# Optimization experiments

Measured on AMD Instinct MI355X. Metric: run time of the kernel, lower is better.

The kernel has to match this reference:

```python
import jax, jax.numpy as jnp
import numpy as np

IN_SZ, HID_SZ, OUT_SZ, NUM_HEAD = 64, 128, 64, 16
BATCH = 131072


def setup_inputs() -> dict:
    key = jax.random.key(0)
    ks = jax.random.split(key, 5)
    # PyTorch Linear default init: U(-1/sqrt(fan_in), 1/sqrt(fan_in))
    b1lim = 1.0 / np.sqrt(IN_SZ)
    b2lim = 1.0 / np.sqrt(HID_SZ)
    return {
        "x": jax.random.normal(ks[0], (BATCH, IN_SZ), dtype=jnp.float32),
        "W1": jax.random.uniform(ks[1], (NUM_HEAD, IN_SZ, HID_SZ), jnp.float32, -b1lim, b1lim),
        "b1": jax.random.uniform(ks[2], (NUM_HEAD, HID_SZ), jnp.float32, -b1lim, b1lim),
        "W2": jax.random.uniform(ks[3], (NUM_HEAD, HID_SZ, OUT_SZ), jnp.float32, -b2lim, b2lim),
        "b2": jax.random.uniform(ks[4], (NUM_HEAD, OUT_SZ), jnp.float32, -b2lim, b2lim),
    }


def reference(x, W1, b1, W2, b2):
    # All heads as one grouped matmul: [B,in] x [H,in,hid] -> [B,H,hid]
    h = jnp.einsum("bi,hio->bho", x, W1) + b1[None, :, :]
    h = jax.nn.elu(h)
    # [B,H,hid] x [H,hid,out] -> [B,H,out]  (matches torch.stack(...).transpose(0,1))
    out = jnp.einsum("bho,hos->bhs", h, W2) + b2[None, :, :]
    return out
```

## Files before the change

kernel.cpp:

```cpp
#include <hip/hip_runtime.h>
#include <hip/hip_bf16.h>


typedef __attribute__((ext_vector_type(8))) short bf16x8;
typedef __attribute__((ext_vector_type(4))) float f32x4;
typedef __attribute__((ext_vector_type(4))) unsigned int u32x4;

union frag_u { u32x4 u; bf16x8 b; };

#define MFMA16(A, B, C) __builtin_amdgcn_mfma_f32_16x16x32_bf16((A), (B), (C), 0, 0, 0)

__device__ __forceinline__ void split2(float a, float b, unsigned &wh, unsigned &wl) {
  unsigned ua = __float_as_uint(a), ub = __float_as_uint(b);
  unsigned ha = ua & 0xFFFF0000u, hb = ub & 0xFFFF0000u;
  float ra = a - __uint_as_float(ha);
  float rb = b - __uint_as_float(hb);
  wh = (ha >> 16) | hb;
  wl = (__float_as_uint(ra) >> 16) | (__float_as_uint(rb) & 0xFFFF0000u);
}

__global__ __launch_bounds__(256, 2)
void mhmlp_kernel(const float* __restrict__ x, const float* __restrict__ W1,
                  const float* __restrict__ b1, const float* __restrict__ W2,
                  const float* __restrict__ b2, float* __restrict__ out) {
  __shared__ __align__(16) char smem[66560];
  unsigned short* w1h = (unsigned short*)(smem);
  unsigned short* w1l = (unsigned short*)(smem + 16384);
  unsigned short* w2h = (unsigned short*)(smem + 32768);
  unsigned short* w2l = (unsigned short*)(smem + 49152);
  float* b1s = (float*)(smem + 65536);
  float* b2s = (float*)(smem + 66048);

  const int head  = blockIdx.x & 15;
  const int chunk = blockIdx.x >> 4;
  const int tid   = threadIdx.x;
  const int lane  = tid & 63;
  const int wave  = tid >> 6;
  const int q = lane >> 4;
  const int m = lane & 15;

  const float* W1g = W1 + (size_t)head * 64 * 128;
  const float* W2g = W2 + (size_t)head * 128 * 64;
  #pragma unroll
  for (int kk = 0; kk < 4; ++kk) {
    int cid = tid + 256 * kk;
    int l   = cid & 63;
    int fid = cid >> 6;
    int lq = l >> 4, lm = l & 15;
    {
      int s = fid & 1, t = fid >> 1;
      u32x4 hw, lw;
      #pragma unroll
      for (int p = 0; p < 4; ++p) {
        int j0 = 2 * p, j1 = j0 + 1;
        int in0 = 32 * s + 16 * (j0 >> 2) + 4 * lq + (j0 & 3);
        int in1 = 32 * s + 16 * (j1 >> 2) + 4 * lq + (j1 & 3);
        float v0 = W1g[in0 * 128 + 16 * t + lm];
        float v1 = W1g[in1 * 128 + 16 * t + lm];
        unsigned a, b; split2(v0, v1, a, b);
        hw[p] = a; lw[p] = b;
      }
      *(u32x4*)(w1h + cid * 8) = hw;
      *(u32x4*)(w1l + cid * 8) = lw;
    }
    {
      int s = fid & 3, u = fid >> 2;
      u32x4 hw, lw;
      #pragma unroll
      for (int p = 0; p < 4; ++p) {
        int j0 = 2 * p, j1 = j0 + 1;
        int k0 = 32 * s + 16 * (j0 >> 2) + 4 * lq + (j0 & 3);
        int k1 = 32 * s + 16 * (j1 >> 2) + 4 * lq + (j1 & 3);
        float v0 = W2g[k0 * 64 + 16 * u + lm];
        float v1 = W2g[k1 * 64 + 16 * u + lm];
        unsigned a, b; split2(v0, v1, a, b);
        hw[p] = a; lw[p] = b;
      }
      *(u32x4*)(w2h + cid * 8) = hw;
      *(u32x4*)(w2l + cid * 8) = lw;
    }
  }
  if (tid < 128) b1s[tid] = b1[head * 128 + tid];
  if (tid < 64)  b2s[tid] = b2[head * 64 + tid];
  __syncthreads();

  const long rowbase0 = (long)chunk * 4096 + wave * 32;
  for (int it = 0; it < 32; ++it) {
    const long rb = rowbase0 + (long)it * 128;

    frag_u xh[2][2], xl[2][2];
    #pragma unroll
    for (int b = 0; b < 2; ++b) {
      const float* xp = x + (rb + 16 * b + m) * 64 + 4 * q;
      #pragma unroll
      for (int s = 0; s < 2; ++s) {
        #pragma unroll
        for (int c = 0; c < 2; ++c) {
          f32x4 v = *(const f32x4*)(xp + 32 * s + 16 * c);
          unsigned h0, l0, h1, l1;
          split2(v.x, v.y, h0, l0);
          split2(v.z, v.w, h1, l1);
          xh[b][s].u[2 * c] = h0;     xl[b][s].u[2 * c] = l0;
          xh[b][s].u[2 * c + 1] = h1; xl[b][s].u[2 * c + 1] = l1;
        }
      }
    }

    f32x4 acc1[8][2];
    #pragma unroll
    for (int t = 0; t < 8; ++t) {
      f32x4 bv = *(const f32x4*)(b1s + t * 16 + q * 4);
      acc1[t][0] = bv; acc1[t][1] = bv;
    }
    #pragma unroll
    for (int s = 0; s < 2; ++s) {
      #pragma unroll
      for (int t = 0; t < 8; ++t) {
        bf16x8 wh = *(const bf16x8*)(w1h + (t * 2 + s) * 512 + lane * 8);
        bf16x8 wl = *(const bf16x8*)(w1l + (t * 2 + s) * 512 + lane * 8);
        #pragma unroll
        for (int b = 0; b < 2; ++b) {
          acc1[t][b] = MFMA16(wh, xh[b][s].b, acc1[t][b]);
          acc1[t][b] = MFMA16(wl, xh[b][s].b, acc1[t][b]);
          acc1[t][b] = MFMA16(wh, xl[b][s].b, acc1[t][b]);
        }
      }
    }

    frag_u a2h[2][4], a2l[2][4];
    #pragma unroll
    for (int b = 0; b < 2; ++b) {
      #pragma unroll
      for (int s2 = 0; s2 < 4; ++s2) {
        float o[8];
        #pragma unroll
        for (int c = 0; c < 2; ++c) {
          #pragma unroll
          for (int r = 0; r < 4; ++r) {
            float v = acc1[2 * s2 + c][b][r];
            float e = exp2f(v * 1.442695040888963f) - 1.0f;
            o[4 * c + r] = (v > 0.0f) ? v : e;
          }
        }
        #pragma unroll
        for (int p = 0; p < 4; ++p) {
          unsigned th, tl;
          split2(o[2 * p], o[2 * p + 1], th, tl);
          a2h[b][s2].u[p] = th;
          a2l[b][s2].u[p] = tl;
        }
      }
    }

    f32x4 acc2[4][2];
    #pragma unroll
    for (int u = 0; u < 4; ++u) {
      float bval = b2s[u * 16 + m];
      f32x4 bv = {bval, bval, bval, bval};
      acc2[u][0] = bv; acc2[u][1] = bv;
    }
    #pragma unroll
    for (int s2 = 0; s2 < 4; ++s2) {
      #pragma unroll
      for (int u = 0; u < 4; ++u) {
        bf16x8 wh = *(const bf16x8*)(w2h + (u * 4 + s2) * 512 + lane * 8);
        bf16x8 wl = *(const bf16x8*)(w2l + (u * 4 + s2) * 512 + lane * 8);
        #pragma unroll
        for (int b = 0; b < 2; ++b) {
          acc2[u][b] = MFMA16(a2h[b][s2].b, wh, acc2[u][b]);
          acc2[u][b] = MFMA16(a2l[b][s2].b, wh, acc2[u][b]);
          acc2[u][b] = MFMA16(a2h[b][s2].b, wl, acc2[u][b]);
        }
      }
    }

    #pragma unroll
    for (int b = 0; b < 2; ++b) {
      #pragma unroll
      for (int r = 0; r < 4; ++r) {
        long row = rb + 16 * b + 4 * q + r;
        float* op = out + (row * 16 + head) * 64 + m;
        #pragma unroll
        for (int u = 0; u < 4; ++u) op[16 * u] = acc2[u][b][r];
      }
    }
  }
}

extern "C" void kernel_launch(void* const* d_in, const int* in_sizes, int n_in,
                              void* d_out, int out_size, void* d_ws, size_t ws_size,
                              hipStream_t stream) {
  const float* x  = (const float*)d_in[0];
  const float* W1 = (const float*)d_in[1];
  const float* b1 = (const float*)d_in[2];
  const float* W2 = (const float*)d_in[3];
  const float* b2 = (const float*)d_in[4];
  float* out = (float*)d_out;
  int batch  = in_sizes[0] / 64;
  int chunks = batch / 4096;
  mhmlp_kernel<<<dim3(16 * chunks), dim3(256), 0, stream>>>(x, W1, b1, W2, b2, out);
}
```

Before: 997.7 us.

## Transpose second GEMM for vectorized nontemporal stores, use 512-thread blocks with XCD remap

Swaps the operand order of the second-layer MFMAs so each lane holds four consecutive output columns, which allows 16-byte nontemporal stores in place of scattered scalar stores. Blocks grow to 512 threads (8 waves) and the grid is fixed at 512, with block indices remapped so that each XCD processes contiguous batch chunks across all heads, improving L2 reuse of x. The hi/lo bf16 split now rounds to nearest-even instead of truncating, for accuracy. Risks: the grid is hardcoded and only fits batch 131072, launch bounds of 512 threads with 4 blocks per CU may force register spills, and 66KB of LDS per block limits occupancy.

```diff
diff --git a/kernel.cpp b/kernel.cpp
--- a/kernel.cpp
+++ b/kernel.cpp
@@ -10,16 +10,20 @@
 
 #define MFMA16(A, B, C) __builtin_amdgcn_mfma_f32_16x16x32_bf16((A), (B), (C), 0, 0, 0)
 
+__device__ __forceinline__ unsigned rne_hi(float a) {
+  unsigned ua = __float_as_uint(a);
+  return (ua + 0x7FFFu + ((ua >> 16) & 1u)) & 0xFFFF0000u;
+}
+
 __device__ __forceinline__ void split2(float a, float b, unsigned &wh, unsigned &wl) {
-  unsigned ua = __float_as_uint(a), ub = __float_as_uint(b);
-  unsigned ha = ua & 0xFFFF0000u, hb = ub & 0xFFFF0000u;
+  unsigned ha = rne_hi(a), hb = rne_hi(b);
   float ra = a - __uint_as_float(ha);
   float rb = b - __uint_as_float(hb);
   wh = (ha >> 16) | hb;
   wl = (__float_as_uint(ra) >> 16) | (__float_as_uint(rb) & 0xFFFF0000u);
 }
 
-__global__ __launch_bounds__(256, 2)
+__global__ __launch_bounds__(512, 4)
 void mhmlp_kernel(const float* __restrict__ x, const float* __restrict__ W1,
                   const float* __restrict__ b1, const float* __restrict__ W2,
                   const float* __restrict__ b2, float* __restrict__ out) {
@@ -31,8 +35,11 @@
   float* b1s = (float*)(smem + 65536);
   float* b2s = (float*)(smem + 66048);
 
-  const int head  = blockIdx.x & 15;
-  const int chunk = blockIdx.x >> 4;
+  const int wid  = blockIdx.x;
+  const int xcd  = wid & 7;
+  const int idx  = wid >> 3;
+  const int head  = idx & 15;
+  const int chunk = xcd + 8 * (idx >> 4);
   const int tid   = threadIdx.x;
   const int lane  = tid & 63;
   const int wave  = tid >> 6;
@@ -42,8 +49,8 @@
   const float* W1g = W1 + (size_t)head * 64 * 128;
   const float* W2g = W2 + (size_t)head * 128 * 64;
   #pragma unroll
-  for (int kk = 0; kk < 4; ++kk) {
-    int cid = tid + 256 * kk;
+  for (int kk = 0; kk < 2; ++kk) {
+    int cid = tid + 512 * kk;
     int l   = cid & 63;
     int fid = cid >> 6;
     int lq = l >> 4, lm = l & 15;
@@ -85,8 +92,8 @@
   __syncthreads();
 
   const long rowbase0 = (long)chunk * 4096 + wave * 32;
-  for (int it = 0; it < 32; ++it) {
-    const long rb = rowbase0 + (long)it * 128;
+  for (int it = 0; it < 16; ++it) {
+    const long rb = rowbase0 + (long)it * 256;
 
     frag_u xh[2][2], xl[2][2];
     #pragma unroll
@@ -155,8 +162,7 @@
     f32x4 acc2[4][2];
     #pragma unroll
     for (int u = 0; u < 4; ++u) {
-      float bval = b2s[u * 16 + m];
-      f32x4 bv = {bval, bval, bval, bval};
+      f32x4 bv = *(const f32x4*)(b2s + u * 16 + q * 4);
       acc2[u][0] = bv; acc2[u][1] = bv;
     }
     #pragma unroll
@@ -167,21 +173,19 @@
         bf16x8 wl = *(const bf16x8*)(w2l + (u * 4 + s2) * 512 + lane * 8);
         #pragma unroll
         for (int b = 0; b < 2; ++b) {
-          acc2[u][b] = MFMA16(a2h[b][s2].b, wh, acc2[u][b]);
-          acc2[u][b] = MFMA16(a2l[b][s2].b, wh, acc2[u][b]);
-          acc2[u][b] = MFMA16(a2h[b][s2].b, wl, acc2[u][b]);
+          acc2[u][b] = MFMA16(wh, a2h[b][s2].b, acc2[u][b]);
+          acc2[u][b] = MFMA16(wh, a2l[b][s2].b, acc2[u][b]);
+          acc2[u][b] = MFMA16(wl, a2h[b][s2].b, acc2[u][b]);
         }
       }
     }
 
     #pragma unroll
     for (int b = 0; b < 2; ++b) {
-      #pragma unroll
-      for (int r = 0; r < 4; ++r) {
-        long row = rb + 16 * b + 4 * q + r;
-        float* op = out + (row * 16 + head) * 64 + m;
-        #pragma unroll
-        for (int u = 0; u < 4; ++u) op[16 * u] = acc2[u][b][r];
+      float* op = out + ((rb + 16 * b + m) * 16 + head) * 64 + 4 * q;
+      #pragma unroll
+      for (int u = 0; u < 4; ++u) {
+        __builtin_nontemporal_store(acc2[u][b], (f32x4*)(op + 16 * u));
       }
     }
   }
@@ -196,7 +200,5 @@
   const float* W2 = (const float*)d_in[3];
   const float* b2 = (const float*)d_in[4];
   float* out = (float*)d_out;
-  int batch  = in_sizes[0] / 64;
-  int chunks = batch / 4096;
-  mhmlp_kernel<<<dim3(16 * chunks), dim3(256), 0, stream>>>(x, W1, b1, W2, b2, out);
-}
+  mhmlp_kernel<<<dim3(512), dim3(512), 0, stream>>>(x, W1, b1, W2, b2, out);
+}
```

Result: slower. 1.558 ms (+56.2%).
